# Kernel tuning notes

Hardware: AMD Instinct MI355X
Metric: run time of the kernel (lower is better)

## Reference

```python
import jax, jax.numpy as jnp
import numpy as np
from jax import lax

PC_RANGE = (-54.0, -54.0, -5.0, 54.0, 54.0, 3.0)
HEIGHTS = (-1.0, 0.0, 1.0)  # all within [z_min, z_max]
IMG_H, IMG_W = 256.0, 704.0  # batch_input_shape of the camera image
BN_EPS = 1e-5


def setup_inputs() -> dict:
    key = jax.random.key(0)
    ks = jax.random.split(key, 11)
    d = {}
    d['radar_bev'] = jax.random.normal(ks[0], (2, 384, 180, 180), jnp.float32)
    d['img_feat'] = jax.random.normal(ks[1], (2, 256, 64, 176), jnp.float32)
    d['lidar2img'] = jax.random.normal(ks[2], (2, 3, 4), jnp.float32)
    d['w1'] = jax.random.normal(ks[3], (384, 256, 1, 1), jnp.float32) * 0.05
    d['bn1'] = jax.random.uniform(ks[4], (4, 384), jnp.float32, 0.1, 1.0)
    d['w2'] = jax.random.normal(ks[5], (384, 384, 3, 3), jnp.float32) * 0.02
    d['bn2'] = jax.random.uniform(ks[6], (4, 384), jnp.float32, 0.1, 1.0)
    d['wf1'] = jax.random.normal(ks[7], (384, 768, 3, 3), jnp.float32) * 0.02
    d['bnf1'] = jax.random.uniform(ks[8], (4, 384), jnp.float32, 0.1, 1.0)
    d['wf2'] = jax.random.normal(ks[9], (384, 384, 3, 3), jnp.float32) * 0.02
    d['bnf2'] = jax.random.uniform(ks[10], (4, 384), jnp.float32, 0.1, 1.0)
    return d


def _conv(x, w, pad):
    return lax.conv_general_dilated(x, w, (1, 1), [(pad, pad), (pad, pad)],
                                    dimension_numbers=('NCHW', 'OIHW', 'NCHW'))


def _bn_relu(x, p):
    g, b, m, v = p[0], p[1], p[2], p[3]
    y = (x - m[:, None, None]) * (g[:, None, None] / jnp.sqrt(v[:, None, None] + BN_EPS)) + b[:, None, None]
    return jax.nn.relu(y)


def _bilinear_sample(img, gx, gy):
    # img: [C,H,W]; gx,gy: [N] normalized coords in grid_sample convention
    # (align_corners=False, padding_mode='zeros')
    C, H, W = img.shape
    ix = ((gx + 1.0) * W - 1.0) * 0.5
    iy = ((gy + 1.0) * H - 1.0) * 0.5
    x0 = jnp.floor(ix); y0 = jnp.floor(iy)
    wx1 = ix - x0; wx0 = 1.0 - wx1
    wy1 = iy - y0; wy0 = 1.0 - wy1

    def corner(xc, yc, w):
        inb = (xc >= 0) & (xc < W) & (yc >= 0) & (yc < H)
        xi = jnp.clip(xc, 0, W - 1).astype(jnp.int32)
        yi = jnp.clip(yc, 0, H - 1).astype(jnp.int32)
        return img[:, yi, xi] * (w * inb)[None, :]

    return (corner(x0, y0, wx0 * wy0) + corner(x0 + 1, y0, wx1 * wy0)
            + corner(x0, y0 + 1, wx0 * wy1) + corner(x0 + 1, y0 + 1, wx1 * wy1))


def reference(radar_bev, img_feat, lidar2img, w1, bn1, w2, bn2, wf1, bnf1, wf2, bnf2):
    B, _, bev_h, bev_w = radar_bev.shape
    x_min, y_min, z_min, x_max, y_max, z_max = PC_RANGE
    xs = jnp.linspace(x_min, x_max, bev_w + 1, dtype=jnp.float32)[:-1] + (x_max - x_min) / bev_w * 0.5
    ys = jnp.linspace(y_min, y_max, bev_h + 1, dtype=jnp.float32)[:-1] + (y_max - y_min) / bev_h * 0.5
    gy, gx = jnp.meshgrid(ys, xs, indexing='ij')  # [bev_h, bev_w]
    zs = jnp.asarray(HEIGHTS, jnp.float32)
    Z = zs.shape[0]
    # points: [Z, bev_h, bev_w, 4] -> [N, 4]
    pts = jnp.stack([jnp.broadcast_to(gx, (Z, bev_h, bev_w)),
                     jnp.broadcast_to(gy, (Z, bev_h, bev_w)),
                     jnp.broadcast_to(zs[:, None, None], (Z, bev_h, bev_w)),
                     jnp.ones((Z, bev_h, bev_w), jnp.float32)], axis=-1).reshape(-1, 4)
    # project: [B, N, 3]
    proj = jnp.einsum('nk,bjk->bnj', pts, lidar2img)
    depth = jnp.maximum(proj[:, :, 2], 1e-5)
    px = proj[:, :, 0] / depth
    py = proj[:, :, 1] / depth
    norm_x = px / IMG_W * 2.0 - 1.0
    norm_y = py / IMG_H * 2.0 - 1.0
    sampled = jax.vmap(_bilinear_sample)(img_feat, norm_x, norm_y)  # [B, C, N]
    valid = ((px >= 0) & (px < IMG_W) & (py >= 0) & (py < IMG_H)
             & (proj[:, :, 2] > 1e-5)).astype(jnp.float32)  # [B, N]
    C = img_feat.shape[1]
    sampled = sampled.reshape(B, C, Z, bev_h, bev_w)
    valid = valid.reshape(B, 1, Z, bev_h, bev_w)
    image_bev = (sampled * valid).sum(axis=2) / jnp.maximum(valid.sum(axis=2), 1.0)
    # image_bev_encoder: 1x1 conv -> BN -> ReLU -> 3x3 conv -> BN -> ReLU
    h = _bn_relu(_conv(image_bev, w1, 0), bn1)
    h = _bn_relu(_conv(h, w2, 1), bn2)
    # bev_fusion on concat(radar, image_bev)
    f = jnp.concatenate([radar_bev, h], axis=1)
    f = _bn_relu(_conv(f, wf1, 1), bnf1)
    f = _bn_relu(_conv(f, wf2, 1), bnf2)
    return f
```

## Files before the change

### kernel.cpp

```cpp
#include <hip/hip_runtime.h>
#include <hip/hip_bf16.h>

#define BEV 180
#define NPOS (BEV * BEV)
#define MTOT (2 * NPOS)
#define IH 64
#define IW 176
#define CIMG 256

typedef __attribute__((ext_vector_type(8))) short bf16x8;
typedef __attribute__((ext_vector_type(4))) float f32x4;

__device__ __forceinline__ void gload_lds16(const void* g, void* l) {
  __builtin_amdgcn_global_load_lds(
      (const __attribute__((address_space(1))) void*)g,
      (__attribute__((address_space(3))) void*)l, 16, 0, 0);
}

__global__ void k_zero(unsigned long long* p) { p[threadIdx.x] = 0ULL; }

template <typename OT>
__device__ __forceinline__ OT conv_out(float v);
template <>
__device__ __forceinline__ float conv_out<float>(float v) { return v; }
template <>
__device__ __forceinline__ __hip_bfloat16 conv_out<__hip_bfloat16>(float v) { return __float2bfloat16(v); }

template <typename OT>
__global__ void k_transpose(const float* __restrict__ in, OT* __restrict__ out, int R, int CL) {
  __shared__ float tile[32][33];
  const float* inb = in + (size_t)blockIdx.z * R * CL;
  OT* outb = out + (size_t)blockIdx.z * R * CL;
  int c0 = blockIdx.x * 32, r0 = blockIdx.y * 32;
  int tx = threadIdx.x, ty = threadIdx.y;
#pragma unroll
  for (int i = 0; i < 32; i += 8) {
    int r = r0 + ty + i, c = c0 + tx;
    tile[ty + i][tx] = (r < R && c < CL) ? inb[(size_t)r * CL + c] : 0.f;
  }
  __syncthreads();
#pragma unroll
  for (int i = 0; i < 32; i += 8) {
    int c = c0 + ty + i, r = r0 + tx;
    if (c < CL && r < R) outb[(size_t)c * R + r] = conv_out<OT>(tile[tx][ty + i]);
  }
}

__global__ void k_sample(const float* __restrict__ imgT, const float* __restrict__ l2i,
                         __hip_bfloat16* __restrict__ out) {
  int blk = blockIdx.x;
  int b = blk / NPOS, rem = blk - b * NPOS;
  int hy = rem / BEV, wx = rem - hy * BEV;
  int c = threadIdx.x;
  float gx = -54.f + 0.3f + 0.6f * (float)wx;
  float gy = -54.f + 0.3f + 0.6f * (float)hy;
  const float* L = l2i + b * 12;
  const float* img = imgT + (size_t)b * (IH * IW * CIMG);
  float acc = 0.f, vcnt = 0.f;
#pragma unroll
  for (int zi = 0; zi < 3; ++zi) {
    float z = (float)(zi - 1);
    float p0 = L[0] * gx + L[1] * gy + L[2] * z + L[3];
    float p1 = L[4] * gx + L[5] * gy + L[6] * z + L[7];
    float p2 = L[8] * gx + L[9] * gy + L[10] * z + L[11];
    float d = fmaxf(p2, 1e-5f);
    float px = p0 / d, py = p1 / d;
    if (px >= 0.f && px < 704.f && py >= 0.f && py < 256.f && p2 > 1e-5f) {
      vcnt += 1.f;
      float ix = px * 0.25f - 0.5f, iy = py * 0.25f - 0.5f;
      float xf = floorf(ix), yf = floorf(iy);
      float wx1 = ix - xf, wy1 = iy - yf;
      float wx0 = 1.f - wx1, wy0 = 1.f - wy1;
      int x0 = (int)xf, y0 = (int)yf;
      int x1 = x0 + 1, y1 = y0 + 1;
      bool bx0 = (unsigned)x0 < IW, bx1 = (unsigned)x1 < IW;
      bool by0 = (unsigned)y0 < IH, by1 = (unsigned)y1 < IH;
      float s = 0.f;
      if (bx0 && by0) s += wx0 * wy0 * img[((size_t)y0 * IW + x0) * CIMG + c];
      if (bx1 && by0) s += wx1 * wy0 * img[((size_t)y0 * IW + x1) * CIMG + c];
      if (bx0 && by1) s += wx0 * wy1 * img[((size_t)y1 * IW + x0) * CIMG + c];
      if (bx1 && by1) s += wx1 * wy1 * img[((size_t)y1 * IW + x1) * CIMG + c];
      acc += s;
    }
  }
  out[(size_t)blk * CIMG + c] = __float2bfloat16(acc / fmaxf(vcnt, 1.f));
}

__global__ void k_packw(const float* __restrict__ w, __hip_bfloat16* __restrict__ wp,
                        int Co, int Ci, int T) {
  size_t idx = (size_t)blockIdx.x * 256 + threadIdx.x;
  size_t tot = (size_t)Co * Ci * T;
  if (idx >= tot) return;
  int ci = (int)(idx % Ci);
  size_t r = idx / Ci;
  int co = (int)(r % Co);
  int tap = (int)(r / Co);
  wp[idx] = __float2bfloat16(w[((size_t)co * Ci + ci) * T + tap]);
}

__global__ void k_packbn(const float* __restrict__ bn, float* __restrict__ sb, int C) {
  int i = blockIdx.x * blockDim.x + threadIdx.x;
  if (i >= C) return;
  float g = bn[i], b = bn[C + i], m = bn[2 * C + i], v = bn[3 * C + i];
  float s = g / sqrtf(v + 1e-5f);
  sb[i] = s;
  sb[C + i] = b - m * s;
}

__global__ __launch_bounds__(256, 2) void k_conv(
    const __hip_bfloat16* __restrict__ x0, const __hip_bfloat16* __restrict__ x1,
    int cin0, int cin1,
    const __hip_bfloat16* __restrict__ wp, const float* __restrict__ sb,
    int taps, int isFinal,
    __hip_bfloat16* __restrict__ obf, float* __restrict__ of32,
    const __hip_bfloat16* __restrict__ zp) {
  const int Cout = 384;
  __shared__ __hip_bfloat16 As[352 * 64];
  __shared__ __hip_bfloat16 Bs[2][128 * 64];
  const int t = threadIdx.x;
  const int w = t >> 6, l = t & 63;
  const int bid = blockIdx.x;
  const int b = bid / 144;
  const int rr = bid - b * 144;
  const int y0 = (rr / 12) * 16;
  const int x0c = (rr - (rr / 12) * 12) * 16;
  const int n0 = blockIdx.y * 128;
  const int cinTot = cin0 + cin1;
  const size_t tapStride = (size_t)Cout * cinTot * 2;
  const int nA0 = cin0 >> 6, nA1 = cin1 >> 6, nA = nA0 + nA1;
  const int P = nA * taps;

  const int baseRow = t >> 3;
  const int cb = ((t & 7) ^ (baseRow & 7)) * 16;
  int posIdx[11];
  unsigned okMask = 0;
#pragma unroll
  for (int j = 0; j < 11; ++j) {
    int row = j * 32 + baseRow;
    int yy = row / 18, xx = row - yy * 18;
    int ys = y0 - 1 + yy, xg = x0c - 1 + xx;
    if (row < 324 && (unsigned)ys < 180u && (unsigned)xg < 180u) okMask |= (1u << j);
    posIdx[j] = b * NPOS + ys * BEV + xg;
  }
  size_t bOff[4];
#pragma unroll
  for (int j = 0; j < 4; ++j)
    bOff[j] = (size_t)(n0 + j * 32 + baseRow) * (size_t)(cinTot * 2) + (size_t)cb;

  auto issueA = [&](int kc) {
    int s1 = (kc >= nA0);
    int kcw = kc - (s1 ? nA0 : 0);
    const char* xb = s1 ? (const char*)x1 : (const char*)x0;
    size_t cinB = (size_t)(s1 ? cin1 : cin0) * 2;
    size_t ko = (size_t)kcw * 128 + (size_t)cb;
    char* dst = (char*)As + w * 1024;
#pragma unroll
    for (int j = 0; j < 11; ++j) {
      const char* src = ((okMask >> j) & 1) ? (xb + (size_t)posIdx[j] * cinB + ko)
                                            : (const char*)zp;
      gload_lds16(src, dst + j * 4096);
    }
  };
  auto issueB = [&](int q, int kc, int tq) {
    int s1 = (kc >= nA0);
    int kcw = kc - (s1 ? nA0 : 0);
    int segoff = s1 ? cin0 : 0;
    const char* wt = (const char*)wp + (size_t)tq * tapStride + (size_t)(segoff + kcw * 64) * 2;
    char* dst = (char*)Bs[q & 1] + w * 1024;
#pragma unroll
    for (int j = 0; j < 4; ++j) gload_lds16(wt + bOff[j], dst + j * 4096);
  };

  f32x4 acc[8][4];
#pragma unroll
  for (int mi = 0; mi < 8; ++mi)
#pragma unroll
    for (int ni = 0; ni < 4; ++ni) acc[mi][ni] = f32x4{0.f, 0.f, 0.f, 0.f};

  const int wq = w >> 1;
  const int wn = (w & 1) * 64;
  const int xl = l & 15, kq = l >> 4;

  issueA(0);
  issueB(0, 0, 0);

  int kc = 0, tap = 0;
  for (int p = 0; p < P; ++p) {
    if (p + 1 < P) {
      int tq = tap + 1, kn = kc;
      if (tq == taps) { tq = 0; ++kn; }
      issueB(p + 1, kn, tq);
      asm volatile("s_waitcnt vmcnt(4)" ::: "memory");
    } else {
      asm volatile("s_waitcnt vmcnt(0)" ::: "memory");
    }
    __builtin_amdgcn_s_barrier();
    asm volatile("" ::: "memory");

    const int dy = (taps == 9) ? (tap / 3 - 1) : 0;
    const int dx = (taps == 9) ? (tap - (tap / 3) * 3 - 1) : 0;
    const int sRow0 = (wq * 8 + dy + 1) * 18 + xl + dx + 1;
    const char* bLds = (const char*)Bs[p & 1];
    __builtin_amdgcn_s_setprio(1);
#pragma unroll
    for (int ks = 0; ks < 2; ++ks) {
      const int g = ks * 4 + kq;
      bf16x8 af[8], bfr[4];
#pragma unroll
      for (int mi = 0; mi < 8; ++mi) {
        int s = sRow0 + mi * 18;
        af[mi] = *(const bf16x8*)((const char*)As + s * 128 + ((g ^ (s & 7)) * 16));
      }
#pragma unroll
      for (int ni = 0; ni < 4; ++ni) {
        int rB = wn + ni * 16 + xl;
        bfr[ni] = *(const bf16x8*)(bLds + rB * 128 + ((g ^ (rB & 7)) * 16));
      }
#pragma unroll
      for (int mi = 0; mi < 8; ++mi)
#pragma unroll
        for (int ni = 0; ni < 4; ++ni)
          acc[mi][ni] = __builtin_amdgcn_mfma_f32_16x16x32_bf16(af[mi], bfr[ni], acc[mi][ni], 0, 0, 0);
    }
    __builtin_amdgcn_s_setprio(0);
    asm volatile("" ::: "memory");
    __builtin_amdgcn_s_barrier();

    if (tap == taps - 1 && kc + 1 < nA) issueA(kc + 1);
    if (++tap == taps) { tap = 0; ++kc; }
  }

  float sc[4], bi[4];
#pragma unroll
  for (int ni = 0; ni < 4; ++ni) {
    int cc = n0 + wn + ni * 16 + xl;
    sc[ni] = sb[cc];
    bi[ni] = sb[Cout + cc];
  }
#pragma unroll
  for (int mi = 0; mi < 8; ++mi) {
    int y = y0 + wq * 8 + mi;
    if (y >= BEV) continue;
#pragma unroll
    for (int j = 0; j < 4; ++j) {
      int x = x0c + kq * 4 + j;
      if (x >= BEV) continue;
      int pp = b * NPOS + y * BEV + x;
#pragma unroll
      for (int ni = 0; ni < 4; ++ni) {
        int cc = n0 + wn + ni * 16 + xl;
        float v = fmaxf(acc[mi][ni][j] * sc[ni] + bi[ni], 0.f);
        if (isFinal) {
          of32[((size_t)(b * Cout + cc)) * NPOS + (size_t)y * BEV + x] = v;
        } else {
          obf[(size_t)pp * Cout + cc] = __float2bfloat16(v);
        }
      }
    }
  }
}

extern "C" void kernel_launch(void* const* d_in, const int* in_sizes, int n_in,
                              void* d_out, int out_size, void* d_ws, size_t ws_size,
                              hipStream_t stream) {
  const float* radar = (const float*)d_in[0];
  const float* imgf = (const float*)d_in[1];
  const float* l2i = (const float*)d_in[2];
  const float* w1 = (const float*)d_in[3];
  const float* bn1 = (const float*)d_in[4];
  const float* w2 = (const float*)d_in[5];
  const float* bn2 = (const float*)d_in[6];
  const float* wf1 = (const float*)d_in[7];
  const float* bnf1 = (const float*)d_in[8];
  const float* wf2 = (const float*)d_in[9];
  const float* bnf2 = (const float*)d_in[10];

  char* ws = (char*)d_ws;
  size_t off = 0;
  auto alloc = [&](size_t bytes) {
    char* p = ws + off;
    off += (bytes + 255) & ~(size_t)255;
    return p;
  };
  char* zp = alloc(4096);
  char* imgT = alloc((size_t)2 * IH * IW * CIMG * 4);
  char* ibev = alloc((size_t)MTOT * CIMG * 2);
  char* radarT = imgT;
  char* h1 = alloc((size_t)MTOT * 384 * 2);
  char* h2 = alloc((size_t)MTOT * 384 * 2);
  char* f1 = h1;
  char* wp1 = alloc((size_t)1 * 384 * 256 * 2);
  char* wp2 = alloc((size_t)9 * 384 * 384 * 2);
  char* wpf1 = alloc((size_t)9 * 384 * 768 * 2);
  char* wpf2 = alloc((size_t)9 * 384 * 384 * 2);
  char* sb1 = alloc(2 * 384 * 4);
  char* sb2 = alloc(2 * 384 * 4);
  char* sbf1 = alloc(2 * 384 * 4);
  char* sbf2 = alloc(2 * 384 * 4);

  k_zero<<<1, 512, 0, stream>>>((unsigned long long*)zp);

  dim3 tb(32, 8);
  k_transpose<float><<<dim3((IH * IW + 31) / 32, (CIMG + 31) / 32, 2), tb, 0, stream>>>(
      imgf, (float*)imgT, CIMG, IH * IW);

  auto packw = [&](const float* src, char* dst, int Co, int Ci, int T) {
    size_t tot = (size_t)Co * Ci * T;
    k_packw<<<(unsigned)((tot + 255) / 256), 256, 0, stream>>>(src, (__hip_bfloat16*)dst, Co, Ci, T);
  };
  packw(w1, wp1, 384, 256, 1);
  packw(w2, wp2, 384, 384, 9);
  packw(wf1, wpf1, 384, 768, 9);
  packw(wf2, wpf2, 384, 384, 9);
  k_packbn<<<2, 256, 0, stream>>>(bn1, (float*)sb1, 384);
  k_packbn<<<2, 256, 0, stream>>>(bn2, (float*)sb2, 384);
  k_packbn<<<2, 256, 0, stream>>>(bnf1, (float*)sbf1, 384);
  k_packbn<<<2, 256, 0, stream>>>(bnf2, (float*)sbf2, 384);

  k_sample<<<MTOT, 256, 0, stream>>>((const float*)imgT, l2i, (__hip_bfloat16*)ibev);

  dim3 cg(288, 3);
  k_conv<<<cg, 256, 0, stream>>>((const __hip_bfloat16*)ibev, nullptr, 256, 0,
                                 (const __hip_bfloat16*)wp1, (const float*)sb1, 1, 0,
                                 (__hip_bfloat16*)h1, nullptr, (const __hip_bfloat16*)zp);
  k_transpose<__hip_bfloat16><<<dim3((NPOS + 31) / 32, (384 + 31) / 32, 2), tb, 0, stream>>>(
      radar, (__hip_bfloat16*)radarT, 384, NPOS);
  k_conv<<<cg, 256, 0, stream>>>((const __hip_bfloat16*)h1, nullptr, 384, 0,
                                 (const __hip_bfloat16*)wp2, (const float*)sb2, 9, 0,
                                 (__hip_bfloat16*)h2, nullptr, (const __hip_bfloat16*)zp);
  k_conv<<<cg, 256, 0, stream>>>((const __hip_bfloat16*)radarT, (const __hip_bfloat16*)h2, 384, 384,
                                 (const __hip_bfloat16*)wpf1, (const float*)sbf1, 9, 0,
                                 (__hip_bfloat16*)f1, nullptr, (const __hip_bfloat16*)zp);
  k_conv<<<cg, 256, 0, stream>>>((const __hip_bfloat16*)f1, nullptr, 384, 0,
                                 (const __hip_bfloat16*)wpf2, (const float*)sbf2, 9, 1,
                                 nullptr, (float*)d_out, (const __hip_bfloat16*)zp);
}
```

Baseline: 940.0 us.

## Load conv weights directly from global into registers, templatize tap count

Removes the double-buffered LDS staging of weight tiles. Each lane now reads its B fragments directly from global memory (L2-cached) into registers, and the tap count becomes a template parameter so the tap loop is fully unrolled. The intent is to cut LDS traffic and per-tap barriers so that only one barrier pair per input-channel chunk remains. The cost is that A tile loads are no longer prefetched: each chunk loads A and waits on vmcnt(0). Global weight loads also sit on the MFMA critical path with higher latency, and register pressure rises.

```diff
diff --git a/kernel.cpp b/kernel.cpp
--- a/kernel.cpp
+++ b/kernel.cpp
@@ -107,16 +107,16 @@
   sb[C + i] = b - m * s;
 }
 
+template <int TAPS>
 __global__ __launch_bounds__(256, 2) void k_conv(
     const __hip_bfloat16* __restrict__ x0, const __hip_bfloat16* __restrict__ x1,
     int cin0, int cin1,
     const __hip_bfloat16* __restrict__ wp, const float* __restrict__ sb,
-    int taps, int isFinal,
+    int isFinal,
     __hip_bfloat16* __restrict__ obf, float* __restrict__ of32,
     const __hip_bfloat16* __restrict__ zp) {
   const int Cout = 384;
   __shared__ __hip_bfloat16 As[352 * 64];
-  __shared__ __hip_bfloat16 Bs[2][128 * 64];
   const int t = threadIdx.x;
   const int w = t >> 6, l = t & 63;
   const int bid = blockIdx.x;
@@ -128,7 +128,6 @@
   const int cinTot = cin0 + cin1;
   const size_t tapStride = (size_t)Cout * cinTot * 2;
   const int nA0 = cin0 >> 6, nA1 = cin1 >> 6, nA = nA0 + nA1;
-  const int P = nA * taps;
 
   const int baseRow = t >> 3;
   const int cb = ((t & 7) ^ (baseRow & 7)) * 16;
@@ -142,11 +141,6 @@
     if (row < 324 && (unsigned)ys < 180u && (unsigned)xg < 180u) okMask |= (1u << j);
     posIdx[j] = b * NPOS + ys * BEV + xg;
   }
-  size_t bOff[4];
-#pragma unroll
-  for (int j = 0; j < 4; ++j)
-    bOff[j] = (size_t)(n0 + j * 32 + baseRow) * (size_t)(cinTot * 2) + (size_t)cb;
-
   auto issueA = [&](int kc) {
     int s1 = (kc >= nA0);
     int kcw = kc - (s1 ? nA0 : 0);
@@ -161,73 +155,64 @@
       gload_lds16(src, dst + j * 4096);
     }
   };
-  auto issueB = [&](int q, int kc, int tq) {
-    int s1 = (kc >= nA0);
-    int kcw = kc - (s1 ? nA0 : 0);
-    int segoff = s1 ? cin0 : 0;
-    const char* wt = (const char*)wp + (size_t)tq * tapStride + (size_t)(segoff + kcw * 64) * 2;
-    char* dst = (char*)Bs[q & 1] + w * 1024;
-#pragma unroll
-    for (int j = 0; j < 4; ++j) gload_lds16(wt + bOff[j], dst + j * 4096);
-  };
-
-  f32x4 acc[8][4];
-#pragma unroll
-  for (int mi = 0; mi < 8; ++mi)
-#pragma unroll
-    for (int ni = 0; ni < 4; ++ni) acc[mi][ni] = f32x4{0.f, 0.f, 0.f, 0.f};
 
   const int wq = w >> 1;
   const int wn = (w & 1) * 64;
   const int xl = l & 15, kq = l >> 4;
 
-  issueA(0);
-  issueB(0, 0, 0);
-
-  int kc = 0, tap = 0;
-  for (int p = 0; p < P; ++p) {
-    if (p + 1 < P) {
-      int tq = tap + 1, kn = kc;
-      if (tq == taps) { tq = 0; ++kn; }
-      issueB(p + 1, kn, tq);
-      asm volatile("s_waitcnt vmcnt(4)" ::: "memory");
-    } else {
-      asm volatile("s_waitcnt vmcnt(0)" ::: "memory");
+  const char* bBase[4];
+#pragma unroll
+  for (int ni = 0; ni < 4; ++ni)
+    bBase[ni] = (const char*)wp + (size_t)(n0 + wn + ni * 16 + xl) * (size_t)(cinTot * 2)
+                + (size_t)(kq * 16);
+
+  f32x4 acc[8][4];
+#pragma unroll
+  for (int mi = 0; mi < 8; ++mi)
+#pragma unroll
+    for (int ni = 0; ni < 4; ++ni) acc[mi][ni] = f32x4{0.f, 0.f, 0.f, 0.f};
+
+  for (int kc = 0; kc < nA; ++kc) {
+    __builtin_amdgcn_s_barrier();
+    issueA(kc);
+    asm volatile("s_waitcnt vmcnt(0)" ::: "memory");
+    __builtin_amdgcn_s_barrier();
+    int s1 = (kc >= nA0);
+    int kcw = kc - (s1 ? nA0 : 0);
+    const size_t kByte = (size_t)((s1 ? cin0 : 0) + kcw * 64) * 2;
+
+#pragma unroll
+    for (int tap = 0; tap < TAPS; ++tap) {
+      asm volatile("" ::: "memory");
+      const size_t kOff = (size_t)tap * tapStride + kByte;
+      bf16x8 bfr[2][4];
+#pragma unroll
+      for (int ks = 0; ks < 2; ++ks)
+#pragma unroll
+        for (int ni = 0; ni < 4; ++ni)
+          bfr[ks][ni] = *(const bf16x8*)(bBase[ni] + kOff + ks * 64);
+
+      const int dy = (TAPS == 9) ? (tap / 3 - 1) : 0;
+      const int dx = (TAPS == 9) ? (tap - (tap / 3) * 3 - 1) : 0;
+      const int sRow0 = (wq * 8 + dy + 1) * 18 + xl + dx + 1;
+      __builtin_amdgcn_s_setprio(1);
+#pragma unroll
+      for (int ks = 0; ks < 2; ++ks) {
+        const int g = ks * 4 + kq;
+        bf16x8 af[8];
+#pragma unroll
+        for (int mi = 0; mi < 8; ++mi) {
+          int s = sRow0 + mi * 18;
+          af[mi] = *(const bf16x8*)((const char*)As + s * 128 + ((g ^ (s & 7)) * 16));
+        }
+#pragma unroll
+        for (int mi = 0; mi < 8; ++mi)
+#pragma unroll
+          for (int ni = 0; ni < 4; ++ni)
+            acc[mi][ni] = __builtin_amdgcn_mfma_f32_16x16x32_bf16(af[mi], bfr[ks][ni], acc[mi][ni], 0, 0, 0);
+      }
+      __builtin_amdgcn_s_setprio(0);
     }
-    __builtin_amdgcn_s_barrier();
-    asm volatile("" ::: "memory");
-
-    const int dy = (taps == 9) ? (tap / 3 - 1) : 0;
-    const int dx = (taps == 9) ? (tap - (tap / 3) * 3 - 1) : 0;
-    const int sRow0 = (wq * 8 + dy + 1) * 18 + xl + dx + 1;
-    const char* bLds = (const char*)Bs[p & 1];
-    __builtin_amdgcn_s_setprio(1);
-#pragma unroll
-    for (int ks = 0; ks < 2; ++ks) {
-      const int g = ks * 4 + kq;
-      bf16x8 af[8], bfr[4];
-#pragma unroll
-      for (int mi = 0; mi < 8; ++mi) {
-        int s = sRow0 + mi * 18;
-        af[mi] = *(const bf16x8*)((const char*)As + s * 128 + ((g ^ (s & 7)) * 16));
-      }
-#pragma unroll
-      for (int ni = 0; ni < 4; ++ni) {
-        int rB = wn + ni * 16 + xl;
-        bfr[ni] = *(const bf16x8*)(bLds + rB * 128 + ((g ^ (rB & 7)) * 16));
-      }
-#pragma unroll
-      for (int mi = 0; mi < 8; ++mi)
-#pragma unroll
-        for (int ni = 0; ni < 4; ++ni)
-          acc[mi][ni] = __builtin_amdgcn_mfma_f32_16x16x32_bf16(af[mi], bfr[ni], acc[mi][ni], 0, 0, 0);
-    }
-    __builtin_amdgcn_s_setprio(0);
-    asm volatile("" ::: "memory");
-    __builtin_amdgcn_s_barrier();
-
-    if (tap == taps - 1 && kc + 1 < nA) issueA(kc + 1);
-    if (++tap == taps) { tap = 0; ++kc; }
   }
 
   float sc[4], bi[4];
@@ -320,18 +305,18 @@
   k_sample<<<MTOT, 256, 0, stream>>>((const float*)imgT, l2i, (__hip_bfloat16*)ibev);
 
   dim3 cg(288, 3);
-  k_conv<<<cg, 256, 0, stream>>>((const __hip_bfloat16*)ibev, nullptr, 256, 0,
-                                 (const __hip_bfloat16*)wp1, (const float*)sb1, 1, 0,
-                                 (__hip_bfloat16*)h1, nullptr, (const __hip_bfloat16*)zp);
+  k_conv<1><<<cg, 256, 0, stream>>>((const __hip_bfloat16*)ibev, nullptr, 256, 0,
+                                    (const __hip_bfloat16*)wp1, (const float*)sb1, 0,
+                                    (__hip_bfloat16*)h1, nullptr, (const __hip_bfloat16*)zp);
   k_transpose<__hip_bfloat16><<<dim3((NPOS + 31) / 32, (384 + 31) / 32, 2), tb, 0, stream>>>(
       radar, (__hip_bfloat16*)radarT, 384, NPOS);
-  k_conv<<<cg, 256, 0, stream>>>((const __hip_bfloat16*)h1, nullptr, 384, 0,
-                                 (const __hip_bfloat16*)wp2, (const float*)sb2, 9, 0,
-                                 (__hip_bfloat16*)h2, nullptr, (const __hip_bfloat16*)zp);
-  k_conv<<<cg, 256, 0, stream>>>((const __hip_bfloat16*)radarT, (const __hip_bfloat16*)h2, 384, 384,
-                                 (const __hip_bfloat16*)wpf1, (const float*)sbf1, 9, 0,
-                                 (__hip_bfloat16*)f1, nullptr, (const __hip_bfloat16*)zp);
-  k_conv<<<cg, 256, 0, stream>>>((const __hip_bfloat16*)f1, nullptr, 384, 0,
-                                 (const __hip_bfloat16*)wpf2, (const float*)sbf2, 9, 1,
-                                 nullptr, (float*)d_out, (const __hip_bfloat16*)zp);
-}
+  k_conv<9><<<cg, 256, 0, stream>>>((const __hip_bfloat16*)h1, nullptr, 384, 0,
+                                    (const __hip_bfloat16*)wp2, (const float*)sb2, 0,
+                                    (__hip_bfloat16*)h2, nullptr, (const __hip_bfloat16*)zp);
+  k_conv<9><<<cg, 256, 0, stream>>>((const __hip_bfloat16*)radarT, (const __hip_bfloat16*)h2, 384, 384,
+                                    (const __hip_bfloat16*)wpf1, (const float*)sbf1, 0,
+                                    (__hip_bfloat16*)f1, nullptr, (const __hip_bfloat16*)zp);
+  k_conv<9><<<cg, 256, 0, stream>>>((const __hip_bfloat16*)f1, nullptr, 384, 0,
+                                    (const __hip_bfloat16*)wpf2, (const float*)sbf2, 1,
+                                    nullptr, (float*)d_out, (const __hip_bfloat16*)zp);
+}
```

After: 1.484 ms. 57.8% more time.

## Enlarge conv spatial tile to 32x16 with 512-thread blocks

Applied to the files above, without the earlier changes.

The conv block now covers 32 rows by 16 columns with 8 waves, so each weight tile loaded into LDS serves twice as many output positions and the 3x3 halo overhead per output shrinks. The tap count becomes a template parameter so the tap arithmetic is resolved at compile time. LDS use per block rises to about 112 KB and the block count halves, which may limit occupancy. The epilogue row mapping (wq*8+mi) is unchanged, so it relies on w>>1 now spanning four row groups.

```diff
diff --git a/kernel.cpp b/kernel.cpp
--- a/kernel.cpp
+++ b/kernel.cpp
@@ -107,45 +107,48 @@
   sb[C + i] = b - m * s;
 }
 
-__global__ __launch_bounds__(256, 2) void k_conv(
+template <int TAPS>
+__global__ __launch_bounds__(512, 2) void k_conv(
     const __hip_bfloat16* __restrict__ x0, const __hip_bfloat16* __restrict__ x1,
     int cin0, int cin1,
     const __hip_bfloat16* __restrict__ wp, const float* __restrict__ sb,
-    int taps, int isFinal,
+    int isFinal,
     __hip_bfloat16* __restrict__ obf, float* __restrict__ of32,
     const __hip_bfloat16* __restrict__ zp) {
   const int Cout = 384;
-  __shared__ __hip_bfloat16 As[352 * 64];
+  __shared__ __hip_bfloat16 As[640 * 64];
   __shared__ __hip_bfloat16 Bs[2][128 * 64];
   const int t = threadIdx.x;
   const int w = t >> 6, l = t & 63;
   const int bid = blockIdx.x;
-  const int b = bid / 144;
-  const int rr = bid - b * 144;
-  const int y0 = (rr / 12) * 16;
+  const int b = bid / 72;
+  const int rr = bid - b * 72;
+  const int y0 = (rr / 12) * 32;
   const int x0c = (rr - (rr / 12) * 12) * 16;
   const int n0 = blockIdx.y * 128;
   const int cinTot = cin0 + cin1;
   const size_t tapStride = (size_t)Cout * cinTot * 2;
   const int nA0 = cin0 >> 6, nA1 = cin1 >> 6, nA = nA0 + nA1;
-  const int P = nA * taps;
+  const int P = nA * TAPS;
 
   const int baseRow = t >> 3;
   const int cb = ((t & 7) ^ (baseRow & 7)) * 16;
-  int posIdx[11];
+  int posIdx[10];
   unsigned okMask = 0;
 #pragma unroll
-  for (int j = 0; j < 11; ++j) {
-    int row = j * 32 + baseRow;
+  for (int j = 0; j < 10; ++j) {
+    int row = j * 64 + baseRow;
     int yy = row / 18, xx = row - yy * 18;
     int ys = y0 - 1 + yy, xg = x0c - 1 + xx;
-    if (row < 324 && (unsigned)ys < 180u && (unsigned)xg < 180u) okMask |= (1u << j);
+    if (row < 612 && (unsigned)ys < 180u && (unsigned)xg < 180u) okMask |= (1u << j);
     posIdx[j] = b * NPOS + ys * BEV + xg;
   }
-  size_t bOff[4];
-#pragma unroll
-  for (int j = 0; j < 4; ++j)
-    bOff[j] = (size_t)(n0 + j * 32 + baseRow) * (size_t)(cinTot * 2) + (size_t)cb;
+  size_t bOff[2];
+#pragma unroll
+  for (int j = 0; j < 2; ++j) {
+    int rB = j * 64 + baseRow;
+    bOff[j] = (size_t)(n0 + rB) * (size_t)(cinTot * 2) + (size_t)cb;
+  }
 
   auto issueA = [&](int kc) {
     int s1 = (kc >= nA0);
@@ -155,10 +158,10 @@
     size_t ko = (size_t)kcw * 128 + (size_t)cb;
     char* dst = (char*)As + w * 1024;
 #pragma unroll
-    for (int j = 0; j < 11; ++j) {
+    for (int j = 0; j < 10; ++j) {
       const char* src = ((okMask >> j) & 1) ? (xb + (size_t)posIdx[j] * cinB + ko)
                                             : (const char*)zp;
-      gload_lds16(src, dst + j * 4096);
+      gload_lds16(src, dst + j * 8192);
     }
   };
   auto issueB = [&](int q, int kc, int tq) {
@@ -168,7 +171,7 @@
     const char* wt = (const char*)wp + (size_t)tq * tapStride + (size_t)(segoff + kcw * 64) * 2;
     char* dst = (char*)Bs[q & 1] + w * 1024;
 #pragma unroll
-    for (int j = 0; j < 4; ++j) gload_lds16(wt + bOff[j], dst + j * 4096);
+    for (int j = 0; j < 2; ++j) gload_lds16(wt + bOff[j], dst + j * 8192);
   };
 
   f32x4 acc[8][4];
@@ -188,17 +191,17 @@
   for (int p = 0; p < P; ++p) {
     if (p + 1 < P) {
       int tq = tap + 1, kn = kc;
-      if (tq == taps) { tq = 0; ++kn; }
+      if (tq == TAPS) { tq = 0; ++kn; }
       issueB(p + 1, kn, tq);
-      asm volatile("s_waitcnt vmcnt(4)" ::: "memory");
+      asm volatile("s_waitcnt vmcnt(2)" ::: "memory");
     } else {
       asm volatile("s_waitcnt vmcnt(0)" ::: "memory");
     }
     __builtin_amdgcn_s_barrier();
     asm volatile("" ::: "memory");
 
-    const int dy = (taps == 9) ? (tap / 3 - 1) : 0;
-    const int dx = (taps == 9) ? (tap - (tap / 3) * 3 - 1) : 0;
+    const int dy = (TAPS == 9) ? (tap / 3 - 1) : 0;
+    const int dx = (TAPS == 9) ? (tap - (tap / 3) * 3 - 1) : 0;
     const int sRow0 = (wq * 8 + dy + 1) * 18 + xl + dx + 1;
     const char* bLds = (const char*)Bs[p & 1];
     __builtin_amdgcn_s_setprio(1);
@@ -226,8 +229,8 @@
     asm volatile("" ::: "memory");
     __builtin_amdgcn_s_barrier();
 
-    if (tap == taps - 1 && kc + 1 < nA) issueA(kc + 1);
-    if (++tap == taps) { tap = 0; ++kc; }
+    if (tap == TAPS - 1 && kc + 1 < nA) issueA(kc + 1);
+    if (++tap == TAPS) { tap = 0; ++kc; }
   }
 
   float sc[4], bi[4];
@@ -319,19 +322,19 @@
 
   k_sample<<<MTOT, 256, 0, stream>>>((const float*)imgT, l2i, (__hip_bfloat16*)ibev);
 
-  dim3 cg(288, 3);
-  k_conv<<<cg, 256, 0, stream>>>((const __hip_bfloat16*)ibev, nullptr, 256, 0,
-                                 (const __hip_bfloat16*)wp1, (const float*)sb1, 1, 0,
-                                 (__hip_bfloat16*)h1, nullptr, (const __hip_bfloat16*)zp);
+  dim3 cg(144, 3);
+  k_conv<1><<<cg, 512, 0, stream>>>((const __hip_bfloat16*)ibev, nullptr, 256, 0,
+                                    (const __hip_bfloat16*)wp1, (const float*)sb1, 0,
+                                    (__hip_bfloat16*)h1, nullptr, (const __hip_bfloat16*)zp);
   k_transpose<__hip_bfloat16><<<dim3((NPOS + 31) / 32, (384 + 31) / 32, 2), tb, 0, stream>>>(
       radar, (__hip_bfloat16*)radarT, 384, NPOS);
-  k_conv<<<cg, 256, 0, stream>>>((const __hip_bfloat16*)h1, nullptr, 384, 0,
-                                 (const __hip_bfloat16*)wp2, (const float*)sb2, 9, 0,
-                                 (__hip_bfloat16*)h2, nullptr, (const __hip_bfloat16*)zp);
-  k_conv<<<cg, 256, 0, stream>>>((const __hip_bfloat16*)radarT, (const __hip_bfloat16*)h2, 384, 384,
-                                 (const __hip_bfloat16*)wpf1, (const float*)sbf1, 9, 0,
-                                 (__hip_bfloat16*)f1, nullptr, (const __hip_bfloat16*)zp);
-  k_conv<<<cg, 256, 0, stream>>>((const __hip_bfloat16*)f1, nullptr, 384, 0,
-                                 (const __hip_bfloat16*)wpf2, (const float*)sbf2, 9, 1,
-                                 nullptr, (float*)d_out, (const __hip_bfloat16*)zp);
-}
+  k_conv<9><<<cg, 512, 0, stream>>>((const __hip_bfloat16*)h1, nullptr, 384, 0,
+                                    (const __hip_bfloat16*)wp2, (const float*)sb2, 0,
+                                    (__hip_bfloat16*)h2, nullptr, (const __hip_bfloat16*)zp);
+  k_conv<9><<<cg, 512, 0, stream>>>((const __hip_bfloat16*)radarT, (const __hip_bfloat16*)h2, 384, 384,
+                                    (const __hip_bfloat16*)wpf1, (const float*)sbf1, 0,
+                                    (__hip_bfloat16*)f1, nullptr, (const __hip_bfloat16*)zp);
+  k_conv<9><<<cg, 512, 0, stream>>>((const __hip_bfloat16*)f1, nullptr, 384, 0,
+                                    (const __hip_bfloat16*)wpf2, (const float*)sbf2, 1,
+                                    nullptr, (float*)d_out, (const __hip_bfloat16*)zp);
+}
```

Result: slower. 1.067 ms (+13.6%).

## Software-pipeline LDS fragment reads with MFMAs and template conv on tap count

Applied to the files above, without the earlier changes.

The conv kernel is templated on the tap count so tap/offset arithmetic becomes compile-time. The inner loop now splits A fragments into two halves with double-buffered registers, interleaving LDS reads with MFMA groups. It also prefetches the next tap's first A fragment during the current tap's last MFMAs, which hides LDS latency behind matrix work. This costs more live registers under launch_bounds(256,2), and the A prefetch relies on the A tile staying in LDS across taps.

```diff
diff --git a/kernel.cpp b/kernel.cpp
--- a/kernel.cpp
+++ b/kernel.cpp
@@ -107,11 +107,12 @@
   sb[C + i] = b - m * s;
 }
 
+template <int TAPS>
 __global__ __launch_bounds__(256, 2) void k_conv(
     const __hip_bfloat16* __restrict__ x0, const __hip_bfloat16* __restrict__ x1,
     int cin0, int cin1,
     const __hip_bfloat16* __restrict__ wp, const float* __restrict__ sb,
-    int taps, int isFinal,
+    int isFinal,
     __hip_bfloat16* __restrict__ obf, float* __restrict__ of32,
     const __hip_bfloat16* __restrict__ zp) {
   const int Cout = 384;
@@ -128,7 +129,7 @@
   const int cinTot = cin0 + cin1;
   const size_t tapStride = (size_t)Cout * cinTot * 2;
   const int nA0 = cin0 >> 6, nA1 = cin1 >> 6, nA = nA0 + nA1;
-  const int P = nA * taps;
+  const int P = nA * TAPS;
 
   const int baseRow = t >> 3;
   const int cb = ((t & 7) ^ (baseRow & 7)) * 16;
@@ -181,14 +182,38 @@
   const int wn = (w & 1) * 64;
   const int xl = l & 15, kq = l >> 4;
 
+  auto rdA = [&](bf16x8* d, int g, int mh, int srow) {
+#pragma unroll
+    for (int m2 = 0; m2 < 4; ++m2) {
+      int s = srow + (mh * 4 + m2) * 18;
+      d[m2] = *(const bf16x8*)((const char*)As + s * 128 + ((g ^ (s & 7)) * 16));
+    }
+  };
+  auto rdB = [&](bf16x8* d, int g, const char* bLds) {
+#pragma unroll
+    for (int ni = 0; ni < 4; ++ni) {
+      int rB = wn + ni * 16 + xl;
+      d[ni] = *(const bf16x8*)(bLds + rB * 128 + ((g ^ (rB & 7)) * 16));
+    }
+  };
+
+#define MFMA16(AF, BF, MH)                                                          \
+  {                                                                                 \
+    _Pragma("unroll") for (int m2 = 0; m2 < 4; ++m2)                                \
+        _Pragma("unroll") for (int ni = 0; ni < 4; ++ni)                            \
+            acc[(MH)*4 + m2][ni] =                                                  \
+        __builtin_amdgcn_mfma_f32_16x16x32_bf16(AF[m2], BF[ni], acc[(MH)*4 + m2][ni], 0, 0, 0); \
+  }
+
   issueA(0);
   issueB(0, 0, 0);
 
+  bf16x8 afc[4], afn[4], bf0[4], bf1[4];
   int kc = 0, tap = 0;
   for (int p = 0; p < P; ++p) {
     if (p + 1 < P) {
       int tq = tap + 1, kn = kc;
-      if (tq == taps) { tq = 0; ++kn; }
+      if (tq == TAPS) { tq = 0; ++kn; }
       issueB(p + 1, kn, tq);
       asm volatile("s_waitcnt vmcnt(4)" ::: "memory");
     } else {
@@ -197,38 +222,37 @@
     __builtin_amdgcn_s_barrier();
     asm volatile("" ::: "memory");
 
-    const int dy = (taps == 9) ? (tap / 3 - 1) : 0;
-    const int dx = (taps == 9) ? (tap - (tap / 3) * 3 - 1) : 0;
+    const int dy = (TAPS == 9) ? (tap / 3 - 1) : 0;
+    const int dx = (TAPS == 9) ? (tap - (tap / 3) * 3 - 1) : 0;
     const int sRow0 = (wq * 8 + dy + 1) * 18 + xl + dx + 1;
     const char* bLds = (const char*)Bs[p & 1];
+
+    if (tap == 0) rdA(afc, kq, 0, sRow0);
+    rdB(bf0, kq, bLds);
+    rdA(afn, kq, 1, sRow0);
+    rdB(bf1, 4 + kq, bLds);
     __builtin_amdgcn_s_setprio(1);
-#pragma unroll
-    for (int ks = 0; ks < 2; ++ks) {
-      const int g = ks * 4 + kq;
-      bf16x8 af[8], bfr[4];
-#pragma unroll
-      for (int mi = 0; mi < 8; ++mi) {
-        int s = sRow0 + mi * 18;
-        af[mi] = *(const bf16x8*)((const char*)As + s * 128 + ((g ^ (s & 7)) * 16));
-      }
-#pragma unroll
-      for (int ni = 0; ni < 4; ++ni) {
-        int rB = wn + ni * 16 + xl;
-        bfr[ni] = *(const bf16x8*)(bLds + rB * 128 + ((g ^ (rB & 7)) * 16));
-      }
-#pragma unroll
-      for (int mi = 0; mi < 8; ++mi)
-#pragma unroll
-        for (int ni = 0; ni < 4; ++ni)
-          acc[mi][ni] = __builtin_amdgcn_mfma_f32_16x16x32_bf16(af[mi], bfr[ni], acc[mi][ni], 0, 0, 0);
-    }
+    MFMA16(afc, bf0, 0);
+    rdA(afc, 4 + kq, 0, sRow0);
+    MFMA16(afn, bf0, 1);
+    rdA(afn, 4 + kq, 1, sRow0);
+    MFMA16(afc, bf1, 0);
+    if (tap + 1 < TAPS) {
+      const int tn = tap + 1;
+      const int dyn = tn / 3 - 1;
+      const int dxn = tn - (tn / 3) * 3 - 1;
+      const int sRowN = (wq * 8 + dyn + 1) * 18 + xl + dxn + 1;
+      rdA(afc, kq, 0, sRowN);
+    }
+    MFMA16(afn, bf1, 1);
     __builtin_amdgcn_s_setprio(0);
     asm volatile("" ::: "memory");
     __builtin_amdgcn_s_barrier();
 
-    if (tap == taps - 1 && kc + 1 < nA) issueA(kc + 1);
-    if (++tap == taps) { tap = 0; ++kc; }
-  }
+    if (tap == TAPS - 1 && kc + 1 < nA) issueA(kc + 1);
+    if (++tap == TAPS) { tap = 0; ++kc; }
+  }
+#undef MFMA16
 
   float sc[4], bi[4];
 #pragma unroll
@@ -320,18 +344,18 @@
   k_sample<<<MTOT, 256, 0, stream>>>((const float*)imgT, l2i, (__hip_bfloat16*)ibev);
 
   dim3 cg(288, 3);
-  k_conv<<<cg, 256, 0, stream>>>((const __hip_bfloat16*)ibev, nullptr, 256, 0,
-                                 (const __hip_bfloat16*)wp1, (const float*)sb1, 1, 0,
-                                 (__hip_bfloat16*)h1, nullptr, (const __hip_bfloat16*)zp);
+  k_conv<1><<<cg, 256, 0, stream>>>((const __hip_bfloat16*)ibev, nullptr, 256, 0,
+                                    (const __hip_bfloat16*)wp1, (const float*)sb1, 0,
+                                    (__hip_bfloat16*)h1, nullptr, (const __hip_bfloat16*)zp);
   k_transpose<__hip_bfloat16><<<dim3((NPOS + 31) / 32, (384 + 31) / 32, 2), tb, 0, stream>>>(
       radar, (__hip_bfloat16*)radarT, 384, NPOS);
-  k_conv<<<cg, 256, 0, stream>>>((const __hip_bfloat16*)h1, nullptr, 384, 0,
-                                 (const __hip_bfloat16*)wp2, (const float*)sb2, 9, 0,
-                                 (__hip_bfloat16*)h2, nullptr, (const __hip_bfloat16*)zp);
-  k_conv<<<cg, 256, 0, stream>>>((const __hip_bfloat16*)radarT, (const __hip_bfloat16*)h2, 384, 384,
-                                 (const __hip_bfloat16*)wpf1, (const float*)sbf1, 9, 0,
-                                 (__hip_bfloat16*)f1, nullptr, (const __hip_bfloat16*)zp);
-  k_conv<<<cg, 256, 0, stream>>>((const __hip_bfloat16*)f1, nullptr, 384, 0,
-                                 (const __hip_bfloat16*)wpf2, (const float*)sbf2, 9, 1,
-                                 nullptr, (float*)d_out, (const __hip_bfloat16*)zp);
-}
+  k_conv<9><<<cg, 256, 0, stream>>>((const __hip_bfloat16*)h1, nullptr, 384, 0,
+                                    (const __hip_bfloat16*)wp2, (const float*)sb2, 0,
+                                    (__hip_bfloat16*)h2, nullptr, (const __hip_bfloat16*)zp);
+  k_conv<9><<<cg, 256, 0, stream>>>((const __hip_bfloat16*)radarT, (const __hip_bfloat16*)h2, 384, 384,
+                                    (const __hip_bfloat16*)wpf1, (const float*)sbf1, 0,
+                                    (__hip_bfloat16*)f1, nullptr, (const __hip_bfloat16*)zp);
+  k_conv<9><<<cg, 256, 0, stream>>>((const __hip_bfloat16*)f1, nullptr, 384, 0,
+                                    (const __hip_bfloat16*)wpf2, (const float*)sbf2, 1,
+                                    nullptr, (float*)d_out, (const __hip_bfloat16*)zp);
+}
```

Result: no change. 939.2 us (-0.1%).
